# Kernel optimization log

Hardware: AMD Instinct MI355X
Metric: run time of the kernel (lower is better)

Reference implementation:

```python
import jax, jax.numpy as jnp
import numpy as np

N, C_IN, C_OUT, H, W = 16, 256, 256, 32, 32
K = 9  # 3x3 kernel


def setup_inputs() -> dict:
    key = jax.random.key(0)
    k1, k2, k3 = jax.random.split(key, 3)
    x = jax.random.normal(k1, (N, C_IN, H, W), dtype=jnp.float32)
    # offsets as produced upstream from anchors: (N, H*W, 18)
    offset = jax.random.normal(k2, (N, H * W, 2 * K), dtype=jnp.float32)
    # DeformConv weight (no bias), kaiming-ish scale
    weight = jax.random.normal(k3, (C_OUT, C_IN, 3, 3), dtype=jnp.float32) * 0.02
    return {"x": x, "offset": offset, "weight": weight}


def _deform_conv3x3(x, offset_nchw, weight):
    """DeformConv v1, kernel 3x3, stride 1, padding 1, dilation 1,
    groups=1, deformable_groups=1, zero padding outside borders."""
    n, c, h, w = x.shape
    o = weight.shape[0]
    # offset channel layout: (dy_k, dx_k) pairs for k = 0..8
    off = offset_nchw.reshape(n, K, 2, h, w)
    dy = off[:, :, 0]  # (N,K,H,W)
    dx = off[:, :, 1]
    ky = (jnp.arange(K) // 3 - 1).astype(x.dtype)  # kernel row offsets -1,0,1
    kx = (jnp.arange(K) % 3 - 1).astype(x.dtype)
    base_y = jnp.arange(h, dtype=x.dtype)[None, None, :, None]
    base_x = jnp.arange(w, dtype=x.dtype)[None, None, None, :]
    py = base_y + ky[None, :, None, None] + dy  # (N,K,H,W) sample rows
    px = base_x + kx[None, :, None, None] + dx  # (N,K,H,W) sample cols

    y0 = jnp.floor(py)
    x0 = jnp.floor(px)
    ly = py - y0  # fractional parts
    lx = px - x0

    x_flat = x.reshape(n, c, h * w)

    def corner(yi, xi, wgt):
        valid = (yi >= 0) & (yi <= h - 1) & (xi >= 0) & (xi <= w - 1)
        yc = jnp.clip(yi, 0, h - 1).astype(jnp.int32)
        xc = jnp.clip(xi, 0, w - 1).astype(jnp.int32)
        idx = (yc * w + xc).reshape(n, K * h * w)
        g = jax.vmap(lambda xf, i: xf[:, i])(x_flat, idx)  # (N,C,K*H*W)
        wv = (wgt * valid.astype(x.dtype)).reshape(n, 1, K * h * w)
        return g * wv

    val = (corner(y0, x0, (1 - ly) * (1 - lx))
           + corner(y0, x0 + 1, (1 - ly) * lx)
           + corner(y0 + 1, x0, ly * (1 - lx))
           + corner(y0 + 1, x0 + 1, ly * lx))
    val = val.reshape(n, c, K, h, w)  # sampled im2col columns
    return jnp.einsum('nckhw,ock->nohw', val, weight.reshape(o, c, K))


def reference(x, offset, weight):
    n, _, h, w = x.shape
    assert h * w == offset.shape[1]
    # AdaptiveConv.forward: (N, HW, 18) -> (N, 18, H, W)
    offset_nchw = jnp.transpose(offset, (0, 2, 1)).reshape(n, 2 * K, h, w)
    return _deform_conv3x3(x, offset_nchw, weight)
```

## Files before the change

kernel.cpp:

```cpp
#include <hip/hip_runtime.h>
#include <hip/hip_bf16.h>

#define NB   16
#define CIN  256
#define COUT 256
#define HH   32
#define WW   32
#define HW   1024
#define KK   9
#define CK   2304

typedef __bf16 bf16x8 __attribute__((ext_vector_type(8)));
typedef float  f32x4  __attribute__((ext_vector_type(4)));

__device__ __forceinline__ unsigned short f2bf(float f) {
    unsigned int u = __float_as_uint(f);
    u += 0x7FFFu + ((u >> 16) & 1u);
    return (unsigned short)(u >> 16);
}
__device__ __forceinline__ float bfhi(unsigned int u) {
    return __uint_as_float(u & 0xFFFF0000u);
}
__device__ __forceinline__ float bflo(unsigned int u) {
    return __uint_as_float(u << 16);
}

__global__ __launch_bounds__(256) void wconv_kernel(const float* __restrict__ w,
                                                    unsigned short* __restrict__ wbf) {
    __shared__ float ls[CK];
    const int o = blockIdx.x;
    const float* wo = w + (size_t)o * CK;
#pragma unroll
    for (int i = threadIdx.x; i < CK; i += 256) ls[i] = wo[i];
    __syncthreads();
    unsigned short* dst = wbf + (size_t)o * CK;
#pragma unroll
    for (int i = threadIdx.x; i < CK; i += 256) {
        int k = i >> 8, c = i & 255;
        dst[i] = f2bf(ls[c * KK + k]);
    }
}

__global__ __launch_bounds__(256) void xt_kernel(const float* __restrict__ x,
                                                 unsigned short* __restrict__ xtb) {
    __shared__ float ls[64][65];
    const int c0  = blockIdx.x * 64;
    const int hw0 = blockIdx.y * 64;
    const int n   = blockIdx.z;
    const int t   = threadIdx.x;
    {
        int c = t >> 2, q = t & 3;
        const float4* base = (const float4*)(x + ((size_t)(n * CIN + c0 + c)) * HW + hw0 + q * 16);
#pragma unroll
        for (int j = 0; j < 4; ++j) {
            float4 v = base[j];
            ls[c][q * 16 + j * 4 + 0] = v.x;
            ls[c][q * 16 + j * 4 + 1] = v.y;
            ls[c][q * 16 + j * 4 + 2] = v.z;
            ls[c][q * 16 + j * 4 + 3] = v.w;
        }
    }
    __syncthreads();
    {
        int hw = t >> 2, seg = (t & 3) * 16;
        unsigned int dw[8];
#pragma unroll
        for (int j = 0; j < 8; ++j) {
            float f0 = ls[seg + 2 * j][hw];
            float f1 = ls[seg + 2 * j + 1][hw];
            dw[j] = (unsigned)f2bf(f0) | ((unsigned)f2bf(f1) << 16);
        }
        uint4* dst = (uint4*)(xtb + ((size_t)(n * HW + hw0 + hw)) * CIN + c0 + seg);
        dst[0] = *(uint4*)&dw[0];
        dst[1] = *(uint4*)&dw[4];
    }
}

__global__ __launch_bounds__(512, 2) void fused_kernel(const unsigned short* __restrict__ wbf,
                                                       const unsigned short* __restrict__ xtb,
                                                       const float* __restrict__ off,
                                                       float* __restrict__ out) {
    __shared__ unsigned short Bs[2][64 * 256];

    const int tid  = threadIdx.x;
    const int wv   = tid >> 6;
    const int lane = tid & 63;
    const int quad = lane >> 4;
    const int l15  = lane & 15;

    const int hwl = tid >> 3;
    const int seg = tid & 7;

    const int id  = blockIdx.x;
    const int n   = ((id & 7) << 1) | ((id >> 3) & 1);
    const int hw0 = (id >> 4) * 64;

    const int hw = hw0 + hwl;
    const int h  = hw >> 5, w = hw & 31;

    const uint4*  xb4  = (const uint4*)(xtb + (size_t)n * HW * CIN);
    const float2* offp = (const float2*)(off + ((size_t)n * HW + hw) * (2 * KK));
    const unsigned short* Abase = wbf + (size_t)(wv * 32 + l15) * CK + quad * 8;

    f32x4 acc[2][4] = {};

    auto setup = [&](float2 o, int tap, float wg[4], int ix[4]) {
        float py = (float)(h + tap / 3 - 1) + o.x;
        float px = (float)(w + tap % 3 - 1) + o.y;
        float y0f = floorf(py), x0f = floorf(px);
        float ly = py - y0f, lx = px - x0f;
        int y0 = (int)y0f, x0 = (int)x0f;
#pragma unroll
        for (int c2 = 0; c2 < 4; ++c2) {
            int yy = y0 + (c2 >> 1);
            int xx = x0 + (c2 & 1);
            float wy = (c2 >> 1) ? ly : 1.0f - ly;
            float wx = (c2 & 1) ? lx : 1.0f - lx;
            bool v = (yy >= 0) && (yy < HH) && (xx >= 0) && (xx < WW);
            wg[c2] = v ? wy * wx : 0.0f;
            int yc = yy < 0 ? 0 : (yy > HH - 1 ? HH - 1 : yy);
            int xc = xx < 0 ? 0 : (xx > WW - 1 ? WW - 1 : xx);
            ix[c2] = yc * WW + xc;
        }
    };

    auto loadc = [&](uint4 cr[16], const int ix[4]) {
#pragma unroll
        for (int s = 0; s < 4; ++s)
#pragma unroll
            for (int c2 = 0; c2 < 4; ++c2)
                cr[s * 4 + c2] = xb4[(size_t)ix[c2] * 32 + s * 8 + seg];
    };

    auto buildB = [&](int nb, int s, const uint4* cr, const float wg[4]) {
        unsigned u0[4], u1[4], u2[4], u3[4];
        *(uint4*)u0 = cr[0]; *(uint4*)u1 = cr[1];
        *(uint4*)u2 = cr[2]; *(uint4*)u3 = cr[3];
        unsigned dw[4];
#pragma unroll
        for (int d = 0; d < 4; ++d) {
            float2 lv;
            lv.x = wg[0] * bflo(u0[d]) + wg[1] * bflo(u1[d])
                 + wg[2] * bflo(u2[d]) + wg[3] * bflo(u3[d]);
            lv.y = wg[0] * bfhi(u0[d]) + wg[1] * bfhi(u1[d])
                 + wg[2] * bfhi(u2[d]) + wg[3] * bfhi(u3[d]);
            __hip_bfloat162 bb = __float22bfloat162_rn(lv);
            dw[d] = *(unsigned*)&bb;
        }
        *(uint4*)&Bs[nb][hwl * 256 + (s * 8 + (seg ^ (hwl & 7))) * 8] = *(uint4*)dw;
    };

    auto mfma_sub = [&](int pb, int s, const bf16x8 af2[2][2]) {
        bf16x8 bfr[4][2];
#pragma unroll
        for (int ni = 0; ni < 4; ++ni)
#pragma unroll
            for (int hh = 0; hh < 2; ++hh) {
                int row = ni * 16 + l15;
                int ch  = s * 8 + ((hh * 4 + quad) ^ (row & 7));
                bfr[ni][hh] = *(const bf16x8*)&Bs[pb][row * 256 + ch * 8];
            }
#pragma unroll
        for (int mi = 0; mi < 2; ++mi)
#pragma unroll
            for (int ni = 0; ni < 4; ++ni) {
                acc[mi][ni] = __builtin_amdgcn_mfma_f32_16x16x32_bf16(af2[mi][0], bfr[ni][0], acc[mi][ni], 0, 0, 0);
                acc[mi][ni] = __builtin_amdgcn_mfma_f32_16x16x32_bf16(af2[mi][1], bfr[ni][1], acc[mi][ni], 0, 0, 0);
            }
    };

    {
        float wg0[4]; int ix0[4]; uint4 cr0[16];
        float2 o0 = offp[0];
        setup(o0, 0, wg0, ix0);
        loadc(cr0, ix0);
#pragma unroll
        for (int s = 0; s < 4; ++s) buildB(0, s, &cr0[s * 4], wg0);
    }
    __syncthreads();

    for (int tap = 0; tap < 9; ++tap) {
        const int pb = tap & 1;

        bf16x8 af[4][2][2];
        {
            const unsigned short* pA = Abase + tap * 256;
#pragma unroll
            for (int s = 0; s < 4; ++s)
#pragma unroll
                for (int mi = 0; mi < 2; ++mi)
#pragma unroll
                    for (int hh = 0; hh < 2; ++hh)
                        af[s][mi][hh] = *(const bf16x8*)(pA + (size_t)mi * 16 * CK + s * 64 + hh * 32);
        }

        float2 onxt;
        if (tap < 8) onxt = offp[tap + 1];

        mfma_sub(pb, 0, af[0]);
        mfma_sub(pb, 1, af[1]);

        float wgn[4]; int ixn[4]; uint4 crs[16];
        if (tap < 8) {
            setup(onxt, tap + 1, wgn, ixn);
            loadc(crs, ixn);
        }

        mfma_sub(pb, 2, af[2]);
        mfma_sub(pb, 3, af[3]);

        if (tap < 8) {
#pragma unroll
            for (int s = 0; s < 4; ++s) buildB(pb ^ 1, s, &crs[s * 4], wgn);
        }
        __syncthreads();
    }

    float* opnt = out + (size_t)n * COUT * HW + hw0;
#pragma unroll
    for (int mi = 0; mi < 2; ++mi)
#pragma unroll
        for (int ni = 0; ni < 4; ++ni) {
            int col = ni * 16 + l15;
#pragma unroll
            for (int rr = 0; rr < 4; ++rr) {
                int row = wv * 32 + mi * 16 + quad * 4 + rr;
                opnt[(size_t)row * HW + col] = acc[mi][ni][rr];
            }
        }
}

extern "C" void kernel_launch(void* const* d_in, const int* in_sizes, int n_in,
                              void* d_out, int out_size, void* d_ws, size_t ws_size,
                              hipStream_t stream) {
    const float* x   = (const float*)d_in[0];
    const float* off = (const float*)d_in[1];
    const float* wt  = (const float*)d_in[2];
    float* out = (float*)d_out;

    unsigned short* wbf = (unsigned short*)d_ws;
    unsigned short* xtb = (unsigned short*)((char*)d_ws + 1179648);

    wconv_kernel<<<256, 256, 0, stream>>>(wt, wbf);
    xt_kernel<<<dim3(4, 16, 16), 256, 0, stream>>>(x, xtb);
    fused_kernel<<<256, 512, 0, stream>>>(wbf, xtb, off, out);
}
```

Measured before the change: 128.9 us.

## Split output channels across two blocks and halve threads per block

The fused deformable-conv kernel now launches 512 blocks of 256 threads, each block computing 128 of the 256 output channels for 64 pixels. Each thread builds two channel segments of the sampled im2col tile. Loads for the second half of the next tap are deferred to reduce live registers. This aims to spread work over more CUs and improve occupancy, at the cost of duplicating the bilinear gather and interpolation work for both channel halves.

```diff
diff --git a/kernel.cpp b/kernel.cpp
--- a/kernel.cpp
+++ b/kernel.cpp
@@ -76,7 +76,7 @@
     }
 }
 
-__global__ __launch_bounds__(512, 2) void fused_kernel(const unsigned short* __restrict__ wbf,
+__global__ __launch_bounds__(256, 2) void fused_kernel(const unsigned short* __restrict__ wbf,
                                                        const unsigned short* __restrict__ xtb,
                                                        const float* __restrict__ off,
                                                        float* __restrict__ out) {
@@ -88,19 +88,20 @@
     const int quad = lane >> 4;
     const int l15  = lane & 15;
 
-    const int hwl = tid >> 3;
-    const int seg = tid & 7;
+    const int hwl  = tid >> 2;
+    const int bseg = tid & 3;
 
     const int id  = blockIdx.x;
     const int n   = ((id & 7) << 1) | ((id >> 3) & 1);
-    const int hw0 = (id >> 4) * 64;
+    const int hw0 = ((id >> 4) & 15) * 64;
+    const int mh  = id >> 8;
 
     const int hw = hw0 + hwl;
     const int h  = hw >> 5, w = hw & 31;
 
     const uint4*  xb4  = (const uint4*)(xtb + (size_t)n * HW * CIN);
     const float2* offp = (const float2*)(off + ((size_t)n * HW + hw) * (2 * KK));
-    const unsigned short* Abase = wbf + (size_t)(wv * 32 + l15) * CK + quad * 8;
+    const unsigned short* Abase = wbf + (size_t)(mh * 128 + wv * 32 + l15) * CK + quad * 8;
 
     f32x4 acc[2][4] = {};
 
@@ -124,30 +125,39 @@
         }
     };
 
-    auto loadc = [&](uint4 cr[16], const int ix[4]) {
-#pragma unroll
-        for (int s = 0; s < 4; ++s)
-#pragma unroll
-            for (int c2 = 0; c2 < 4; ++c2)
-                cr[s * 4 + c2] = xb4[(size_t)ix[c2] * 32 + s * 8 + seg];
-    };
-
-    auto buildB = [&](int nb, int s, const uint4* cr, const float wg[4]) {
-        unsigned u0[4], u1[4], u2[4], u3[4];
-        *(uint4*)u0 = cr[0]; *(uint4*)u1 = cr[1];
-        *(uint4*)u2 = cr[2]; *(uint4*)u3 = cr[3];
-        unsigned dw[4];
-#pragma unroll
-        for (int d = 0; d < 4; ++d) {
-            float2 lv;
-            lv.x = wg[0] * bflo(u0[d]) + wg[1] * bflo(u1[d])
-                 + wg[2] * bflo(u2[d]) + wg[3] * bflo(u3[d]);
-            lv.y = wg[0] * bfhi(u0[d]) + wg[1] * bfhi(u1[d])
-                 + wg[2] * bfhi(u2[d]) + wg[3] * bfhi(u3[d]);
-            __hip_bfloat162 bb = __float22bfloat162_rn(lv);
-            dw[d] = *(unsigned*)&bb;
-        }
-        *(uint4*)&Bs[nb][hwl * 256 + (s * 8 + (seg ^ (hwl & 7))) * 8] = *(uint4*)dw;
+    auto loadc2 = [&](uint4 cr[16], const int ix[4], int s) {
+#pragma unroll
+        for (int ss = 0; ss < 2; ++ss)
+#pragma unroll
+            for (int c2 = 0; c2 < 4; ++c2) {
+                const uint4* rp = xb4 + (size_t)ix[c2] * 32 + (s + ss) * 8 + bseg * 2;
+                cr[ss * 8 + c2 * 2]     = rp[0];
+                cr[ss * 8 + c2 * 2 + 1] = rp[1];
+            }
+    };
+
+    auto buildB2 = [&](int nb, int s, const uint4 cr[16], const float wg[4]) {
+#pragma unroll
+        for (int ss = 0; ss < 2; ++ss)
+#pragma unroll
+            for (int p = 0; p < 2; ++p) {
+                unsigned u0[4], u1[4], u2[4], u3[4];
+                *(uint4*)u0 = cr[ss * 8 + 0 + p]; *(uint4*)u1 = cr[ss * 8 + 2 + p];
+                *(uint4*)u2 = cr[ss * 8 + 4 + p]; *(uint4*)u3 = cr[ss * 8 + 6 + p];
+                unsigned dw[4];
+#pragma unroll
+                for (int d = 0; d < 4; ++d) {
+                    float2 lv;
+                    lv.x = wg[0] * bflo(u0[d]) + wg[1] * bflo(u1[d])
+                         + wg[2] * bflo(u2[d]) + wg[3] * bflo(u3[d]);
+                    lv.y = wg[0] * bfhi(u0[d]) + wg[1] * bfhi(u1[d])
+                         + wg[2] * bfhi(u2[d]) + wg[3] * bfhi(u3[d]);
+                    __hip_bfloat162 bb = __float22bfloat162_rn(lv);
+                    dw[d] = *(unsigned*)&bb;
+                }
+                int ch = (s + ss) * 8 + ((bseg * 2 + p) ^ (hwl & 7));
+                *(uint4*)&Bs[nb][hwl * 256 + ch * 8] = *(uint4*)dw;
+            }
     };
 
     auto mfma_sub = [&](int pb, int s, const bf16x8 af2[2][2]) {
@@ -170,12 +180,12 @@
     };
 
     {
-        float wg0[4]; int ix0[4]; uint4 cr0[16];
-        float2 o0 = offp[0];
-        setup(o0, 0, wg0, ix0);
-        loadc(cr0, ix0);
-#pragma unroll
-        for (int s = 0; s < 4; ++s) buildB(0, s, &cr0[s * 4], wg0);
+        float wg0[4]; int ix0[4]; uint4 cr[16];
+        setup(offp[0], 0, wg0, ix0);
+        loadc2(cr, ix0, 0);
+        buildB2(0, 0, cr, wg0);
+        loadc2(cr, ix0, 2);
+        buildB2(0, 2, cr, wg0);
     }
     __syncthreads();
 
@@ -200,18 +210,20 @@
         mfma_sub(pb, 0, af[0]);
         mfma_sub(pb, 1, af[1]);
 
-        float wgn[4]; int ixn[4]; uint4 crs[16];
+        float wgn[4]; int ixn[4]; uint4 cr01[16];
         if (tap < 8) {
             setup(onxt, tap + 1, wgn, ixn);
-            loadc(crs, ixn);
+            loadc2(cr01, ixn, 0);
         }
 
         mfma_sub(pb, 2, af[2]);
         mfma_sub(pb, 3, af[3]);
 
         if (tap < 8) {
-#pragma unroll
-            for (int s = 0; s < 4; ++s) buildB(pb ^ 1, s, &crs[s * 4], wgn);
+            buildB2(pb ^ 1, 0, cr01, wgn);
+            uint4 cr23[16];
+            loadc2(cr23, ixn, 2);
+            buildB2(pb ^ 1, 2, cr23, wgn);
         }
         __syncthreads();
     }
@@ -224,7 +236,7 @@
             int col = ni * 16 + l15;
 #pragma unroll
             for (int rr = 0; rr < 4; ++rr) {
-                int row = wv * 32 + mi * 16 + quad * 4 + rr;
+                int row = mh * 128 + wv * 32 + mi * 16 + quad * 4 + rr;
                 opnt[(size_t)row * HW + col] = acc[mi][ni][rr];
             }
         }
@@ -243,5 +255,5 @@
 
     wconv_kernel<<<256, 256, 0, stream>>>(wt, wbf);
     xt_kernel<<<dim3(4, 16, 16), 256, 0, stream>>>(x, xtb);
-    fused_kernel<<<256, 512, 0, stream>>>(wbf, xtb, off, out);
-}
+    fused_kernel<<<512, 256, 0, stream>>>(wbf, xtb, off, out);
+}
```

New measurement: 137.1 us. 1.06x slower.
